# Kernel optimization log

Measured on AMD Instinct MI355X. Metric: run time of the kernel, lower is better.

The kernel has to match this reference:

```python
import jax, jax.numpy as jnp
import numpy as np

N = 40000      # total nodes in the batched graph
E = 640000     # total edges (avg degree 16)
F_IN = 1280    # num_features (ESM embedding dim)
H = 128        # hidden_dim
G = 64         # number of graphs in the batch
OUT = 273      # output_dim (GO terms)
NEG_SLOPE = 0.2
BN_EPS = 1e-5


def setup_inputs() -> dict:
    key = jax.random.key(0)
    ks = jax.random.split(key, 16)
    def nrm(k, shape, s=0.05):
        return jax.random.normal(k, shape, dtype=jnp.float32) * s
    inp = {}
    inp["x"] = jax.random.normal(ks[0], (N, F_IN), dtype=jnp.float32)
    inp["edge_index"] = jax.random.randint(ks[1], (2, E), 0, N, dtype=jnp.int32)
    inp["batch"] = jnp.sort(jax.random.randint(ks[2], (N,), 0, G, dtype=jnp.int32))
    inp["W1"] = nrm(ks[3], (F_IN, H)); inp["b1"] = jnp.zeros((H,), jnp.float32)
    inp["a_src1"] = nrm(ks[4], (H,)); inp["a_dst1"] = nrm(ks[5], (H,))
    inp["W2"] = nrm(ks[6], (H, H)); inp["b2"] = jnp.zeros((H,), jnp.float32)
    inp["a_src2"] = nrm(ks[7], (H,)); inp["a_dst2"] = nrm(ks[8], (H,))
    inp["W3"] = nrm(ks[9], (H, H)); inp["b3"] = jnp.zeros((H,), jnp.float32)
    inp["a_src3"] = nrm(ks[10], (H,)); inp["a_dst3"] = nrm(ks[11], (H,))
    inp["fc1_W"] = nrm(ks[12], (H, 1024)); inp["fc1_b"] = jnp.zeros((1024,), jnp.float32)
    inp["bn_g"] = jnp.ones((1024,), jnp.float32); inp["bn_b"] = jnp.zeros((1024,), jnp.float32)
    inp["bn_rm"] = jnp.zeros((1024,), jnp.float32); inp["bn_rv"] = jnp.ones((1024,), jnp.float32)
    inp["fc2_W"] = nrm(ks[13], (1024, OUT)); inp["fc2_b"] = jnp.zeros((OUT,), jnp.float32)
    return inp


def gat_layer(x, W, b, a_src, a_dst, src, dst, n_nodes):
    # single-head GAT ('gat_originated'): h = xW, e_ij = lrelu(a_src.h_j + a_dst.h_i)
    h = x @ W                                            # [N, H]
    e = jax.nn.leaky_relu((h @ a_src)[src] + (h @ a_dst)[dst], NEG_SLOPE)  # [E]
    # numerically-stable segment softmax over incoming edges of each target node
    m = jax.ops.segment_max(e, dst, num_segments=n_nodes)
    p = jnp.exp(e - m[dst])
    denom = jax.ops.segment_sum(p, dst, num_segments=n_nodes)
    alpha = p / (denom[dst] + 1e-16)                     # [E]
    out = jax.ops.segment_sum(alpha[:, None] * h[src], dst, num_segments=n_nodes)
    return out + b


def reference(x, edge_index, batch, W1, b1, a_src1, a_dst1, W2, b2, a_src2, a_dst2,
              W3, b3, a_src3, a_dst3, fc1_W, fc1_b, bn_g, bn_b, bn_rm, bn_rv, fc2_W, fc2_b):
    n = x.shape[0]
    src, dst = edge_index[0], edge_index[1]
    h = jax.nn.relu(gat_layer(x, W1, b1, a_src1, a_dst1, src, dst, n))
    h = jax.nn.relu(gat_layer(h, W2, b2, a_src2, a_dst2, src, dst, n))
    h = gat_layer(h, W3, b3, a_src3, a_dst3, src, dst, n)
    # gap: global mean pool per graph
    cnt = jax.ops.segment_sum(jnp.ones((n,), h.dtype), batch, num_segments=G)
    pooled = jax.ops.segment_sum(h, batch, num_segments=G) / jnp.maximum(cnt, 1.0)[:, None]
    z = pooled @ fc1_W + fc1_b                            # [G, 1024]
    z = (z - bn_rm) * jax.lax.rsqrt(bn_rv + BN_EPS) * bn_g + bn_b  # BN eval mode
    z = jax.nn.relu(z)                                    # dropout is identity in eval
    return jax.nn.sigmoid(z @ fc2_W + fc2_b)              # [G, 273]
```

## Files before the change

kernel.cpp:

```cpp
#include <hip/hip_runtime.h>
#include <math.h>

#define N_NODES 40000
#define N_EDGES 640000
#define F_IN    1280
#define H       128
#define NG      64
#define OUTD    273
#define FC1D    1024
#define NEG_SLOPE 0.2f
#define BN_EPS  1e-5f

typedef __attribute__((ext_vector_type(8))) short short8;
typedef __attribute__((ext_vector_type(4))) float f32x4;

__device__ __forceinline__ unsigned short f2bf(float f) {
    unsigned u = __float_as_uint(f);
    u += 0x7FFF + ((u >> 16) & 1);
    return (unsigned short)(u >> 16);
}
__device__ __forceinline__ float bf2f(unsigned short s) {
    return __uint_as_float((unsigned)s << 16);
}

__global__ void edge_hist(const int* __restrict__ dst, int* __restrict__ cnt, int e) {
    int i = blockIdx.x * blockDim.x + threadIdx.x;
    if (i < e) atomicAdd(&cnt[dst[i]], 1);
}

__global__ void scan_excl(const int* __restrict__ cnt, int* __restrict__ row_ptr, int n) {
    const int CH = 40;
    __shared__ int sm[1024];
    int tid = threadIdx.x;
    int start = tid * CH;
    int local[CH];
    int s = 0;
    #pragma unroll
    for (int k = 0; k < CH; ++k) {
        int i = start + k;
        int v = (i < n) ? cnt[i] : 0;
        local[k] = s;
        s += v;
    }
    sm[tid] = s;
    __syncthreads();
    for (int off = 1; off < 1024; off <<= 1) {
        int t = (tid >= off) ? sm[tid - off] : 0;
        __syncthreads();
        sm[tid] += t;
        __syncthreads();
    }
    int base = sm[tid] - s;
    #pragma unroll
    for (int k = 0; k < CH; ++k) {
        int i = start + k;
        if (i < n) row_ptr[i] = base + local[k];
    }
    if (tid == 1023) row_ptr[n] = sm[1023];
}

__global__ void edge_fill(const int* __restrict__ src, const int* __restrict__ dst,
                          const int* __restrict__ row_ptr, int* __restrict__ fill,
                          int* __restrict__ csr_src, int e) {
    int i = blockIdx.x * blockDim.x + threadIdx.x;
    if (i < e) {
        int d = dst[i];
        int pos = row_ptr[d] + atomicAdd(&fill[d], 1);
        csr_src[pos] = src[i];
    }
}

__device__ __forceinline__ void wprep_one(const float* __restrict__ W,
                                          unsigned short* __restrict__ Bp,
                                          int i, int K) {
    int k = i >> 7, col = i & 127;
    float v = W[i];
    unsigned short hh = f2bf(v);
    unsigned short ll = f2bf(v - bf2f(hh));
    int t = k >> 6, rr = k & 63;
    int s = rr >> 5, r5 = rr & 31;
    int laneHi = r5 >> 3, j = r5 & 7;
    int lane = laneHi * 16 + (col & 15);
    int n = col >> 4;
    int U = (n * 2 + s) * 64 + lane;
    size_t idx = (size_t)t * 16384 + (size_t)U * 8 + j;
    Bp[idx] = hh;
    Bp[idx + 8192] = ll;
}

__global__ void wprep_all(const float* __restrict__ W1, const float* __restrict__ W2,
                          const float* __restrict__ W3, unsigned short* __restrict__ Bp1,
                          unsigned short* __restrict__ Bp2, unsigned short* __restrict__ Bp3) {
    int i = blockIdx.x * blockDim.x + threadIdx.x;
    const int n1 = F_IN * H, n2 = H * H;
    if (i < n1) { wprep_one(W1, Bp1, i, F_IN); return; }
    i -= n1;
    if (i < n2) { wprep_one(W2, Bp2, i, H); return; }
    i -= n2;
    if (i < n2) { wprep_one(W3, Bp3, i, H); }
}

__device__ __forceinline__ void cvt8(float4 x, float4 y, short8& hi, short8& lo) {
    float f[8] = {x.x, x.y, x.z, x.w, y.x, y.y, y.z, y.w};
    #pragma unroll
    for (int j = 0; j < 8; ++j) {
        unsigned u = __float_as_uint(f[j]);
        unsigned short hh = (unsigned short)((u + 0x7FFF + ((u >> 16) & 1)) >> 16);
        hi[j] = (short)hh;
        float r = f[j] - __uint_as_float((unsigned)hh << 16);
        unsigned ur = __float_as_uint(r);
        lo[j] = (short)((ur + 0x7FFF + ((ur >> 16) & 1)) >> 16);
    }
}

__global__ __launch_bounds__(256) void gemm_fused(
    const float* __restrict__ A, const unsigned short* __restrict__ Bp,
    const float* __restrict__ a_src, const float* __restrict__ a_dst,
    unsigned short* __restrict__ hWb, float* __restrict__ hs,
    float* __restrict__ hd, int K)
{
    __shared__ __align__(16) unsigned short lds[16384];
    const int tid  = threadIdx.x;
    const int lane = tid & 63, wv = tid >> 6;
    const int fr = lane & 15, q = lane >> 4;
    const int m0 = blockIdx.x * 64;
    const int row = m0 + wv * 16 + fr;
    const int nt = K >> 6;

    const uint4* gb = (const uint4*)Bp + tid;
    const float* Aptr = A + (size_t)row * K + q * 8;

    f32x4 acc0 = {}, acc1 = {}, acc2 = {}, acc3 = {},
          acc4 = {}, acc5 = {}, acc6 = {}, acc7 = {};

    uint4 bA0, bA1, bA2, bA3, bA4, bA5, bA6, bA7;
    uint4 bB0, bB1, bB2, bB3, bB4, bB5, bB6, bB7;
    float4 aA0, aA1, aA2, aA3, aB0, aB1, aB2, aB3;

#define LOADB(t, r0, r1, r2, r3, r4, r5, r6, r7)                                \
    { const uint4* g = gb + (size_t)(t) * 2048;                                 \
      r0 = g[0];    r1 = g[256];  r2 = g[512];  r3 = g[768];                    \
      r4 = g[1024]; r5 = g[1280]; r6 = g[1536]; r7 = g[1792]; }
#define LOADA(t, x0, x1, x2, x3)                                                \
    { const float* ap = Aptr + (size_t)(t) * 64;                                \
      x0 = *(const float4*)(ap);      x1 = *(const float4*)(ap + 4);            \
      x2 = *(const float4*)(ap + 32); x3 = *(const float4*)(ap + 36); }
#define STAGE(r0, r1, r2, r3, r4, r5, r6, r7)                                   \
    { uint4* lp = (uint4*)lds + tid;                                            \
      lp[0] = r0;    lp[256] = r1;  lp[512] = r2;  lp[768] = r3;                \
      lp[1024] = r4; lp[1280] = r5; lp[1536] = r6; lp[1792] = r7; }
#define MSTEP(nn, accv, ss)                                                     \
    { const short8 bh = *(const short8*)&lds[(size_t)(((nn)*2+(ss))*64 + lane)*8];        \
      const short8 bl = *(const short8*)&lds[(size_t)(((nn)*2+(ss))*64 + lane)*8 + 8192]; \
      accv = __builtin_amdgcn_mfma_f32_16x16x32_bf16(ah, bh, accv, 0, 0, 0);    \
      accv = __builtin_amdgcn_mfma_f32_16x16x32_bf16(ah, bl, accv, 0, 0, 0);    \
      accv = __builtin_amdgcn_mfma_f32_16x16x32_bf16(al, bh, accv, 0, 0, 0); }
#define COMPUTE(x0, x1, x2, x3)                                                 \
    { short8 ah, al;                                                            \
      cvt8(x0, x1, ah, al);                                                     \
      MSTEP(0, acc0, 0) MSTEP(1, acc1, 0) MSTEP(2, acc2, 0)                     \
      MSTEP(3, acc3, 0) MSTEP(4, acc4, 0) MSTEP(5, acc5, 0)                     \
      MSTEP(6, acc6, 0) MSTEP(7, acc7, 0)                                       \
      cvt8(x2, x3, ah, al);                                                     \
      MSTEP(0, acc0, 1) MSTEP(1, acc1, 1) MSTEP(2, acc2, 1)                     \
      MSTEP(3, acc3, 1) MSTEP(4, acc4, 1) MSTEP(5, acc5, 1)                     \
      MSTEP(6, acc6, 1) MSTEP(7, acc7, 1) }

    LOADB(0, bA0, bA1, bA2, bA3, bA4, bA5, bA6, bA7);
    LOADA(0, aA0, aA1, aA2, aA3);

    for (int t = 0; t < nt; t += 2) {
        STAGE(bA0, bA1, bA2, bA3, bA4, bA5, bA6, bA7);
        LOADB(t + 1, bB0, bB1, bB2, bB3, bB4, bB5, bB6, bB7);
        LOADA(t + 1, aB0, aB1, aB2, aB3);
        __syncthreads();
        COMPUTE(aA0, aA1, aA2, aA3);
        __syncthreads();
        STAGE(bB0, bB1, bB2, bB3, bB4, bB5, bB6, bB7);
        if (t + 2 < nt) {
            LOADB(t + 2, bA0, bA1, bA2, bA3, bA4, bA5, bA6, bA7);
            LOADA(t + 2, aA0, aA1, aA2, aA3);
        }
        __syncthreads();
        COMPUTE(aB0, aB1, aB2, aB3);
        __syncthreads();
    }
#undef LOADB
#undef LOADA
#undef STAGE
#undef MSTEP
#undef COMPUTE

    const int rb = m0 + wv * 16 + q * 4;
#define EPI(nn, accv)                                                           \
    {                                                                           \
        _Pragma("unroll")                                                       \
        for (int i = 0; i < 4; ++i)                                             \
            hWb[(size_t)(rb + i) * H + (nn)*16 + fr] = f2bf(accv[i]);           \
    }
    EPI(0, acc0) EPI(1, acc1) EPI(2, acc2) EPI(3, acc3)
    EPI(4, acc4) EPI(5, acc5) EPI(6, acc6) EPI(7, acc7)
#undef EPI

    float asv[8], adv[8];
    #pragma unroll
    for (int n = 0; n < 8; ++n) {
        asv[n] = a_src[n * 16 + fr];
        adv[n] = a_dst[n * 16 + fr];
    }
    #pragma unroll
    for (int i = 0; i < 4; ++i) {
        float ss = acc0[i]*asv[0] + acc1[i]*asv[1] + acc2[i]*asv[2] + acc3[i]*asv[3]
                 + acc4[i]*asv[4] + acc5[i]*asv[5] + acc6[i]*asv[6] + acc7[i]*asv[7];
        float dd = acc0[i]*adv[0] + acc1[i]*adv[1] + acc2[i]*adv[2] + acc3[i]*adv[3]
                 + acc4[i]*adv[4] + acc5[i]*adv[5] + acc6[i]*adv[6] + acc7[i]*adv[7];
        #pragma unroll
        for (int off = 8; off; off >>= 1) {
            ss += __shfl_xor(ss, off);
            dd += __shfl_xor(dd, off);
        }
        if (fr == 0) { hs[rb + i] = ss; hd[rb + i] = dd; }
    }
}

__device__ __forceinline__ float bfhi(unsigned u) { return __uint_as_float(u << 16); }
__device__ __forceinline__ float bflo(unsigned u) { return __uint_as_float(u & 0xffff0000u); }

__global__ void attn_agg(const unsigned short* __restrict__ hWb,
                         const float* __restrict__ hs, const float* __restrict__ hd,
                         const int* __restrict__ row_ptr, const int* __restrict__ csr_src,
                         const float* __restrict__ bias, float* __restrict__ out,
                         int n, int relu_flag) {
    int wv = (blockIdx.x * blockDim.x + threadIdx.x) >> 6;
    int lane = threadIdx.x & 63;
    if (wv >= n) return;
    int p0 = row_ptr[wv], p1 = row_ptr[wv + 1];
    int deg = p1 - p0;
    float hdi = hd[wv];
    float ax = 0.f, ay = 0.f;
    const unsigned* hb = (const unsigned*)hWb;

    if (deg <= 64) {
        int valid = (lane < deg);
        int sidx = valid ? csr_src[p0 + lane] : 0;
        float hsv = hs[sidx];

#define PF(k) int s_##k = __shfl(sidx, k); unsigned u_##k = 0;                  \
              if (deg > k) u_##k = hb[(size_t)s_##k * 64 + lane];
        PF(0)  PF(1)  PF(2)  PF(3)  PF(4)  PF(5)  PF(6)  PF(7)
        PF(8)  PF(9)  PF(10) PF(11) PF(12) PF(13) PF(14) PF(15)
#undef PF

        float e = hsv + hdi;
        e = (e >= 0.f) ? e : NEG_SLOPE * e;
        float m = valid ? e : -3.4e38f;
        #pragma unroll
        for (int off = 32; off; off >>= 1) m = fmaxf(m, __shfl_xor(m, off));
        float pe = valid ? __expf(e - m) : 0.f;
        float dsum = pe;
        #pragma unroll
        for (int off = 32; off; off >>= 1) dsum += __shfl_xor(dsum, off);
        pe *= 1.f / (dsum + 1e-16f);

#define AC(k) if (deg > k) { float aa = __shfl(pe, k);                          \
                             ax += aa * bfhi(u_##k); ay += aa * bflo(u_##k); }
        AC(0)  AC(1)  AC(2)  AC(3)  AC(4)  AC(5)  AC(6)  AC(7)
        AC(8)  AC(9)  AC(10) AC(11) AC(12) AC(13) AC(14) AC(15)
#undef AC

        for (int j = 16; j < deg; j += 4) {
            int t0 = __shfl(sidx, j);
            int t1 = (j + 1 < deg) ? __shfl(sidx, j + 1) : t0;
            int t2 = (j + 2 < deg) ? __shfl(sidx, j + 2) : t0;
            int t3 = (j + 3 < deg) ? __shfl(sidx, j + 3) : t0;
            unsigned v0 = hb[(size_t)t0 * 64 + lane];
            unsigned v1 = hb[(size_t)t1 * 64 + lane];
            unsigned v2 = hb[(size_t)t2 * 64 + lane];
            unsigned v3 = hb[(size_t)t3 * 64 + lane];
            float b0 = __shfl(pe, j);
            float b1 = (j + 1 < deg) ? __shfl(pe, j + 1) : 0.f;
            float b2 = (j + 2 < deg) ? __shfl(pe, j + 2) : 0.f;
            float b3 = (j + 3 < deg) ? __shfl(pe, j + 3) : 0.f;
            ax += b0 * bfhi(v0); ay += b0 * bflo(v0);
            ax += b1 * bfhi(v1); ay += b1 * bflo(v1);
            ax += b2 * bfhi(v2); ay += b2 * bflo(v2);
            ax += b3 * bfhi(v3); ay += b3 * bflo(v3);
        }
    } else {
        float m = -3.4e38f;
        for (int p = p0 + lane; p < p1; p += 64) {
            float e = hs[csr_src[p]] + hdi;
            e = (e >= 0.f) ? e : NEG_SLOPE * e;
            m = fmaxf(m, e);
        }
        #pragma unroll
        for (int off = 32; off; off >>= 1) m = fmaxf(m, __shfl_xor(m, off));
        float dsum = 0.f;
        for (int p = p0 + lane; p < p1; p += 64) {
            float e = hs[csr_src[p]] + hdi;
            e = (e >= 0.f) ? e : NEG_SLOPE * e;
            dsum += __expf(e - m);
        }
        #pragma unroll
        for (int off = 32; off; off >>= 1) dsum += __shfl_xor(dsum, off);
        float inv = 1.f / (dsum + 1e-16f);
        for (int p = p0; p < p1; ++p) {
            int s = csr_src[p];
            float e = hs[s] + hdi;
            e = (e >= 0.f) ? e : NEG_SLOPE * e;
            float alpha = __expf(e - m) * inv;
            unsigned u = hb[(size_t)s * 64 + lane];
            ax += alpha * bfhi(u); ay += alpha * bflo(u);
        }
    }
    float2 bv = *(const float2*)&bias[2 * lane];
    float o0 = ax + bv.x;
    float o1 = ay + bv.y;
    if (relu_flag) { o0 = fmaxf(o0, 0.f); o1 = fmaxf(o1, 0.f); }
    float2 ov; ov.x = o0; ov.y = o1;
    *(float2*)&out[(size_t)wv * H + 2 * lane] = ov;
}

__device__ __forceinline__ void graph_range(const int* __restrict__ batch, int n,
                                            int g, int& start, int& end) {
    int lo = 0, hi = n;
    while (lo < hi) { int mid = (lo + hi) >> 1; if (batch[mid] < g) lo = mid + 1; else hi = mid; }
    start = lo;
    lo = start; hi = n;
    while (lo < hi) { int mid = (lo + hi) >> 1; if (batch[mid] < g + 1) lo = mid + 1; else hi = mid; }
    end = lo;
}

__global__ void pool_part(const float* __restrict__ h, const int* __restrict__ batch,
                          float* __restrict__ part, int n) {
    int g = blockIdx.x >> 3, c = blockIdx.x & 7;
    int f = threadIdx.x;
    int start, end;
    graph_range(batch, n, g, start, end);
    int len = end - start;
    int cs = start + (len * c) / 8, ce = start + (len * (c + 1)) / 8;
    float acc = 0.f;
    for (int i = cs; i < ce; ++i) acc += h[(size_t)i * H + f];
    part[((size_t)g * 8 + c) * H + f] = acc;
}

__global__ void fc1_bn_relu(const float* __restrict__ part, const int* __restrict__ batch,
                            const float* __restrict__ W, const float* __restrict__ b,
                            const float* __restrict__ bng, const float* __restrict__ bnb,
                            const float* __restrict__ bnrm, const float* __restrict__ bnrv,
                            float* __restrict__ z, int n) {
    __shared__ float pr[H];
    int g = blockIdx.x >> 2;
    int tid = threadIdx.x;
    if (tid < H) {
        int start, end;
        graph_range(batch, n, g, start, end);
        float s = 0.f;
        #pragma unroll
        for (int c = 0; c < 8; ++c) s += part[((size_t)g * 8 + c) * H + tid];
        pr[tid] = s / fmaxf((float)(end - start), 1.f);
    }
    __syncthreads();
    int j = ((blockIdx.x & 3) << 8) + tid;
    float acc = b[j];
    #pragma unroll 8
    for (int k = 0; k < H; ++k) acc += pr[k] * W[k * FC1D + j];
    float v = (acc - bnrm[j]) * rsqrtf(bnrv[j] + BN_EPS) * bng[j] + bnb[j];
    z[g * FC1D + j] = fmaxf(v, 0.f);
}

__global__ void fc2_sig(const float* __restrict__ z, const float* __restrict__ W,
                        const float* __restrict__ b, float* __restrict__ out) {
    int g = blockIdx.x;
    int j = threadIdx.x;
    if (j >= OUTD) return;
    const float* zr = z + g * FC1D;
    float acc = b[j];
    #pragma unroll 4
    for (int k = 0; k < FC1D; ++k) acc += zr[k] * W[k * OUTD + j];
    out[g * OUTD + j] = 1.f / (1.f + __expf(-acc));
}

extern "C" void kernel_launch(void* const* d_in, const int* in_sizes, int n_in,
                              void* d_out, int out_size, void* d_ws, size_t ws_size,
                              hipStream_t stream) {
    const float* x     = (const float*)d_in[0];
    const int*   eidx  = (const int*)d_in[1];
    const int*   batch = (const int*)d_in[2];
    const float* W1 = (const float*)d_in[3];  const float* b1 = (const float*)d_in[4];
    const float* as1 = (const float*)d_in[5]; const float* ad1 = (const float*)d_in[6];
    const float* W2 = (const float*)d_in[7];  const float* b2 = (const float*)d_in[8];
    const float* as2 = (const float*)d_in[9]; const float* ad2 = (const float*)d_in[10];
    const float* W3 = (const float*)d_in[11]; const float* b3 = (const float*)d_in[12];
    const float* as3 = (const float*)d_in[13]; const float* ad3 = (const float*)d_in[14];
    const float* fc1W = (const float*)d_in[15]; const float* fc1b = (const float*)d_in[16];
    const float* bng = (const float*)d_in[17];  const float* bnb = (const float*)d_in[18];
    const float* bnrm = (const float*)d_in[19]; const float* bnrv = (const float*)d_in[20];
    const float* fc2W = (const float*)d_in[21]; const float* fc2b = (const float*)d_in[22];
    const int* src = eidx;
    const int* dst = eidx + N_EDGES;

    float* hA      = (float*)d_ws;
    float* hs      = hA + (size_t)N_NODES * H;
    float* hd      = hs + N_NODES;
    float* part    = hd + N_NODES;
    float* z       = part + NG * 8 * H;
    unsigned short* hWb = (unsigned short*)(z + NG * FC1D);
    unsigned short* Bp1 = hWb + (size_t)N_NODES * H;
    unsigned short* Bp2 = Bp1 + (size_t)(F_IN / 64) * 16384;
    unsigned short* Bp3 = Bp2 + (size_t)(H / 64) * 16384;
    int*   row_ptr = (int*)(Bp3 + (size_t)(H / 64) * 16384);
    int*   row_cnt = row_ptr + (N_NODES + 1);
    int*   csr_src = row_cnt + N_NODES;

    const int EB = (N_EDGES + 255) / 256;
    const int NW = (N_NODES * 64 + 255) / 256;
    const int GB = N_NODES / 64;

    const int WTOT = F_IN * H + 2 * H * H;
    wprep_all<<<(WTOT + 255) / 256, 256, 0, stream>>>(W1, W2, W3, Bp1, Bp2, Bp3);

    hipMemsetAsync(row_cnt, 0, N_NODES * sizeof(int), stream);
    edge_hist<<<EB, 256, 0, stream>>>(dst, row_cnt, N_EDGES);
    scan_excl<<<1, 1024, 0, stream>>>(row_cnt, row_ptr, N_NODES);
    hipMemsetAsync(row_cnt, 0, N_NODES * sizeof(int), stream);
    edge_fill<<<EB, 256, 0, stream>>>(src, dst, row_ptr, row_cnt, csr_src, N_EDGES);

    gemm_fused<<<GB, 256, 0, stream>>>(x, Bp1, as1, ad1, hWb, hs, hd, F_IN);
    attn_agg<<<NW, 256, 0, stream>>>(hWb, hs, hd, row_ptr, csr_src, b1, hA, N_NODES, 1);
    gemm_fused<<<GB, 256, 0, stream>>>(hA, Bp2, as2, ad2, hWb, hs, hd, H);
    attn_agg<<<NW, 256, 0, stream>>>(hWb, hs, hd, row_ptr, csr_src, b2, hA, N_NODES, 1);
    gemm_fused<<<GB, 256, 0, stream>>>(hA, Bp3, as3, ad3, hWb, hs, hd, H);
    attn_agg<<<NW, 256, 0, stream>>>(hWb, hs, hd, row_ptr, csr_src, b3, hA, N_NODES, 0);

    pool_part<<<NG * 8, H, 0, stream>>>(hA, batch, part, N_NODES);
    fc1_bn_relu<<<NG * 4, 256, 0, stream>>>(part, batch, fc1W, fc1b, bng, bnb, bnrm, bnrv, z, N_NODES);
    fc2_sig<<<NG, 320, 0, stream>>>(z, fc2W, fc2b, (float*)d_out);
}
```

Measured before the change: 739.0 us.

## Double-buffer GEMM B tiles via direct global-to-LDS loads and fuse memsets

The GEMM now keeps two LDS buffers for the weight tiles and fills them with global_load_lds (direct global-to-LDS DMA) instead of staging through registers. This lets the next tile's load overlap the current tile's MFMA work and cuts the barriers per iteration from four to two. The edge histogram and CSR fill kernels each process four edges per thread using int4 loads. The two hipMemsetAsync calls are removed: zeroing of the histogram counter and a new separate fill counter is folded into the weight-prep kernel. The changes double LDS use per block, which may lower occupancy, and add a new fill buffer to the workspace.

```diff
diff --git a/kernel.cpp b/kernel.cpp
--- a/kernel.cpp
+++ b/kernel.cpp
@@ -23,9 +23,21 @@
     return __uint_as_float((unsigned)s << 16);
 }
 
-__global__ void edge_hist(const int* __restrict__ dst, int* __restrict__ cnt, int e) {
+__device__ __forceinline__ void gll16(const void* g, void* l) {
+    __builtin_amdgcn_global_load_lds(
+        (const __attribute__((address_space(1))) unsigned*)g,
+        (__attribute__((address_space(3))) unsigned*)l, 16, 0, 0);
+}
+
+__global__ void edge_hist(const int* __restrict__ dst, int* __restrict__ cnt, int e4) {
     int i = blockIdx.x * blockDim.x + threadIdx.x;
-    if (i < e) atomicAdd(&cnt[dst[i]], 1);
+    if (i < e4) {
+        int4 d = *(const int4*)(dst + i * 4);
+        atomicAdd(&cnt[d.x], 1);
+        atomicAdd(&cnt[d.y], 1);
+        atomicAdd(&cnt[d.z], 1);
+        atomicAdd(&cnt[d.w], 1);
+    }
 }
 
 __global__ void scan_excl(const int* __restrict__ cnt, int* __restrict__ row_ptr, int n) {
@@ -61,12 +73,16 @@
 
 __global__ void edge_fill(const int* __restrict__ src, const int* __restrict__ dst,
                           const int* __restrict__ row_ptr, int* __restrict__ fill,
-                          int* __restrict__ csr_src, int e) {
+                          int* __restrict__ csr_src, int e4) {
     int i = blockIdx.x * blockDim.x + threadIdx.x;
-    if (i < e) {
-        int d = dst[i];
-        int pos = row_ptr[d] + atomicAdd(&fill[d], 1);
-        csr_src[pos] = src[i];
+    if (i < e4) {
+        int4 sv = *(const int4*)(src + i * 4);
+        int4 dv = *(const int4*)(dst + i * 4);
+        int p;
+        p = row_ptr[dv.x] + atomicAdd(&fill[dv.x], 1); csr_src[p] = sv.x;
+        p = row_ptr[dv.y] + atomicAdd(&fill[dv.y], 1); csr_src[p] = sv.y;
+        p = row_ptr[dv.z] + atomicAdd(&fill[dv.z], 1); csr_src[p] = sv.z;
+        p = row_ptr[dv.w] + atomicAdd(&fill[dv.w], 1); csr_src[p] = sv.w;
     }
 }
 
@@ -90,14 +106,16 @@
 
 __global__ void wprep_all(const float* __restrict__ W1, const float* __restrict__ W2,
                           const float* __restrict__ W3, unsigned short* __restrict__ Bp1,
-                          unsigned short* __restrict__ Bp2, unsigned short* __restrict__ Bp3) {
+                          unsigned short* __restrict__ Bp2, unsigned short* __restrict__ Bp3,
+                          int* __restrict__ row_cnt, int* __restrict__ fill2) {
     int i = blockIdx.x * blockDim.x + threadIdx.x;
+    if (i < N_NODES) { row_cnt[i] = 0; fill2[i] = 0; }
     const int n1 = F_IN * H, n2 = H * H;
     if (i < n1) { wprep_one(W1, Bp1, i, F_IN); return; }
-    i -= n1;
-    if (i < n2) { wprep_one(W2, Bp2, i, H); return; }
-    i -= n2;
-    if (i < n2) { wprep_one(W3, Bp3, i, H); }
+    int i2 = i - n1;
+    if (i2 < n2) { wprep_one(W2, Bp2, i2, H); return; }
+    i2 -= n2;
+    if (i2 < n2) { wprep_one(W3, Bp3, i2, H); }
 }
 
 __device__ __forceinline__ void cvt8(float4 x, float4 y, short8& hi, short8& lo) {
@@ -119,7 +137,7 @@
     unsigned short* __restrict__ hWb, float* __restrict__ hs,
     float* __restrict__ hd, int K)
 {
-    __shared__ __align__(16) unsigned short lds[16384];
+    __shared__ __align__(16) unsigned short lds[2][16384];
     const int tid  = threadIdx.x;
     const int lane = tid & 63, wv = tid >> 6;
     const int fr = lane & 15, q = lane >> 4;
@@ -127,67 +145,60 @@
     const int row = m0 + wv * 16 + fr;
     const int nt = K >> 6;
 
-    const uint4* gb = (const uint4*)Bp + tid;
+    const char* gbB = (const char*)Bp + (size_t)tid * 16;
+    const size_t ldsWv = (size_t)(tid & ~63) * 16;
     const float* Aptr = A + (size_t)row * K + q * 8;
 
     f32x4 acc0 = {}, acc1 = {}, acc2 = {}, acc3 = {},
           acc4 = {}, acc5 = {}, acc6 = {}, acc7 = {};
 
-    uint4 bA0, bA1, bA2, bA3, bA4, bA5, bA6, bA7;
-    uint4 bB0, bB1, bB2, bB3, bB4, bB5, bB6, bB7;
     float4 aA0, aA1, aA2, aA3, aB0, aB1, aB2, aB3;
 
-#define LOADB(t, r0, r1, r2, r3, r4, r5, r6, r7)                                \
-    { const uint4* g = gb + (size_t)(t) * 2048;                                 \
-      r0 = g[0];    r1 = g[256];  r2 = g[512];  r3 = g[768];                    \
-      r4 = g[1024]; r5 = g[1280]; r6 = g[1536]; r7 = g[1792]; }
+#define GLL(t, buf)                                                             \
+    { const char* g = gbB + (size_t)(t) * 32768;                                \
+      char* l = (char*)lds[buf] + ldsWv;                                        \
+      _Pragma("unroll")                                                         \
+      for (int r = 0; r < 8; ++r) gll16(g + r * 4096, l + r * 4096); }
 #define LOADA(t, x0, x1, x2, x3)                                                \
     { const float* ap = Aptr + (size_t)(t) * 64;                                \
       x0 = *(const float4*)(ap);      x1 = *(const float4*)(ap + 4);            \
       x2 = *(const float4*)(ap + 32); x3 = *(const float4*)(ap + 36); }
-#define STAGE(r0, r1, r2, r3, r4, r5, r6, r7)                                   \
-    { uint4* lp = (uint4*)lds + tid;                                            \
-      lp[0] = r0;    lp[256] = r1;  lp[512] = r2;  lp[768] = r3;                \
-      lp[1024] = r4; lp[1280] = r5; lp[1536] = r6; lp[1792] = r7; }
-#define MSTEP(nn, accv, ss)                                                     \
-    { const short8 bh = *(const short8*)&lds[(size_t)(((nn)*2+(ss))*64 + lane)*8];        \
-      const short8 bl = *(const short8*)&lds[(size_t)(((nn)*2+(ss))*64 + lane)*8 + 8192]; \
+#define MSTEP(buf, nn, accv, ss)                                                \
+    { const short8 bh = *(const short8*)&lds[buf][(size_t)(((nn)*2+(ss))*64 + lane)*8];        \
+      const short8 bl = *(const short8*)&lds[buf][(size_t)(((nn)*2+(ss))*64 + lane)*8 + 8192]; \
       accv = __builtin_amdgcn_mfma_f32_16x16x32_bf16(ah, bh, accv, 0, 0, 0);    \
       accv = __builtin_amdgcn_mfma_f32_16x16x32_bf16(ah, bl, accv, 0, 0, 0);    \
       accv = __builtin_amdgcn_mfma_f32_16x16x32_bf16(al, bh, accv, 0, 0, 0); }
-#define COMPUTE(x0, x1, x2, x3)                                                 \
+#define COMPUTE(buf, x0, x1, x2, x3)                                            \
     { short8 ah, al;                                                            \
       cvt8(x0, x1, ah, al);                                                     \
-      MSTEP(0, acc0, 0) MSTEP(1, acc1, 0) MSTEP(2, acc2, 0)                     \
-      MSTEP(3, acc3, 0) MSTEP(4, acc4, 0) MSTEP(5, acc5, 0)                     \
-      MSTEP(6, acc6, 0) MSTEP(7, acc7, 0)                                       \
+      MSTEP(buf, 0, acc0, 0) MSTEP(buf, 1, acc1, 0) MSTEP(buf, 2, acc2, 0)      \
+      MSTEP(buf, 3, acc3, 0) MSTEP(buf, 4, acc4, 0) MSTEP(buf, 5, acc5, 0)      \
+      MSTEP(buf, 6, acc6, 0) MSTEP(buf, 7, acc7, 0)                             \
       cvt8(x2, x3, ah, al);                                                     \
-      MSTEP(0, acc0, 1) MSTEP(1, acc1, 1) MSTEP(2, acc2, 1)                     \
-      MSTEP(3, acc3, 1) MSTEP(4, acc4, 1) MSTEP(5, acc5, 1)                     \
-      MSTEP(6, acc6, 1) MSTEP(7, acc7, 1) }
-
-    LOADB(0, bA0, bA1, bA2, bA3, bA4, bA5, bA6, bA7);
+      MSTEP(buf, 0, acc0, 1) MSTEP(buf, 1, acc1, 1) MSTEP(buf, 2, acc2, 1)      \
+      MSTEP(buf, 3, acc3, 1) MSTEP(buf, 4, acc4, 1) MSTEP(buf, 5, acc5, 1)      \
+      MSTEP(buf, 6, acc6, 1) MSTEP(buf, 7, acc7, 1) }
+
+    GLL(0, 0);
     LOADA(0, aA0, aA1, aA2, aA3);
+    __syncthreads();
 
     for (int t = 0; t < nt; t += 2) {
-        STAGE(bA0, bA1, bA2, bA3, bA4, bA5, bA6, bA7);
-        LOADB(t + 1, bB0, bB1, bB2, bB3, bB4, bB5, bB6, bB7);
+        GLL(t + 1, 1);
         LOADA(t + 1, aB0, aB1, aB2, aB3);
+        COMPUTE(0, aA0, aA1, aA2, aA3);
         __syncthreads();
-        COMPUTE(aA0, aA1, aA2, aA3);
+
+        if (t + 2 < nt) {
+            GLL(t + 2, 0);
+            LOADA(t + 2, aA0, aA1, aA2, aA3);
+        }
+        COMPUTE(1, aB0, aB1, aB2, aB3);
         __syncthreads();
-        STAGE(bB0, bB1, bB2, bB3, bB4, bB5, bB6, bB7);
-        if (t + 2 < nt) {
-            LOADB(t + 2, bA0, bA1, bA2, bA3, bA4, bA5, bA6, bA7);
-            LOADA(t + 2, aA0, aA1, aA2, aA3);
-        }
-        __syncthreads();
-        COMPUTE(aB0, aB1, aB2, aB3);
-        __syncthreads();
-    }
-#undef LOADB
+    }
+#undef GLL
 #undef LOADA
-#undef STAGE
 #undef MSTEP
 #undef COMPUTE
 
@@ -412,19 +423,20 @@
     int*   row_ptr = (int*)(Bp3 + (size_t)(H / 64) * 16384);
     int*   row_cnt = row_ptr + (N_NODES + 1);
     int*   csr_src = row_cnt + N_NODES;
-
-    const int EB = (N_EDGES + 255) / 256;
+    int*   fill2   = csr_src + N_EDGES;
+
+    const int E4 = N_EDGES / 4;
+    const int EB = (E4 + 255) / 256;
     const int NW = (N_NODES * 64 + 255) / 256;
     const int GB = N_NODES / 64;
 
     const int WTOT = F_IN * H + 2 * H * H;
-    wprep_all<<<(WTOT + 255) / 256, 256, 0, stream>>>(W1, W2, W3, Bp1, Bp2, Bp3);
-
-    hipMemsetAsync(row_cnt, 0, N_NODES * sizeof(int), stream);
-    edge_hist<<<EB, 256, 0, stream>>>(dst, row_cnt, N_EDGES);
+    wprep_all<<<(WTOT + 255) / 256, 256, 0, stream>>>(W1, W2, W3, Bp1, Bp2, Bp3,
+                                                      row_cnt, fill2);
+
+    edge_hist<<<EB, 256, 0, stream>>>(dst, row_cnt, E4);
     scan_excl<<<1, 1024, 0, stream>>>(row_cnt, row_ptr, N_NODES);
-    hipMemsetAsync(row_cnt, 0, N_NODES * sizeof(int), stream);
-    edge_fill<<<EB, 256, 0, stream>>>(src, dst, row_ptr, row_cnt, csr_src, N_EDGES);
+    edge_fill<<<EB, 256, 0, stream>>>(src, dst, row_ptr, fill2, csr_src, E4);
 
     gemm_fused<<<GB, 256, 0, stream>>>(x, Bp1, as1, ad1, hWb, hs, hd, F_IN);
     attn_agg<<<NW, 256, 0, stream>>>(hWb, hs, hd, row_ptr, csr_src, b1, hA, N_NODES, 1);
```

Result: no change. 742.2 us (+0.4%).
